# Kernel optimization log

Measured on AMD Instinct MI355X. Metric: run time of the kernel, lower is better.

## Reference

```python
import jax, jax.numpy as jnp
import numpy as np

N_NODES = 100000
N_EDGES = 1600000
EMB_DIM = 128
BN_EPS = 1e-5


def setup_inputs() -> dict:
    key = jax.random.key(0)
    k = jax.random.split(key, 5)
    x = jax.random.normal(k[0], (N_NODES, EMB_DIM), dtype=jnp.float32)
    src = jax.random.randint(k[1], (N_EDGES,), 0, N_NODES)
    dst = jax.random.randint(k[2], (N_EDGES,), 0, N_NODES)
    W = jax.random.normal(k[3], (EMB_DIM, EMB_DIM), dtype=jnp.float32) / np.float32(np.sqrt(EMB_DIM))
    b = jnp.zeros((EMB_DIM,), dtype=jnp.float32)
    gamma = jnp.ones((EMB_DIM,), dtype=jnp.float32)
    beta = jnp.zeros((EMB_DIM,), dtype=jnp.float32)
    return {"x": x, "src": src, "dst": dst, "W": W, "b": b, "gamma": gamma, "beta": beta}


def reference(x, src, dst, W, b, gamma, beta):
    n = x.shape[0]
    ones = jnp.ones(src.shape, dtype=x.dtype)
    # DGL GraphConv norm='both': degrees clamped to min 1
    deg_out = jnp.maximum(jax.ops.segment_sum(ones, src, num_segments=n), 1.0)
    deg_in = jnp.maximum(jax.ops.segment_sum(ones, dst, num_segments=n), 1.0)
    norm_src = jax.lax.rsqrt(deg_out)  # [N]
    norm_dst = jax.lax.rsqrt(deg_in)   # [N]
    # W applied before aggregation (in_feats == out_feats path in DGL)
    h = (x * norm_src[:, None]) @ W                              # [N, D]
    agg = jax.ops.segment_sum(h[src], dst, num_segments=n)       # SpMM gather/scatter, [N, D]
    h = agg * norm_dst[:, None] + b                              # [N, D]
    # BatchNorm1d over nodes (training-mode batch stats, biased variance)
    mean = jnp.mean(h, axis=0)
    var = jnp.var(h, axis=0)
    h = (h - mean) * jax.lax.rsqrt(var + BN_EPS) * gamma + beta
    h = jax.nn.relu(h)
    # dropout: identity in eval-mode reference
    return h + x  # residual
```

## Files before the change

### kernel.cpp

```cpp
#include <hip/hip_runtime.h>
#include <hip/hip_bf16.h>

#define NN 100000
#define NE 1600000
#define D  128
#define BN_EPS 1e-5f

#define CB  782
#define NC  256
#define EPC (NE / NC)
#define NSLICE  2
#define SLICESZ 61600
#define SW      (SLICESZ / 4)
#define SCH     256
#define EPH (NE / SCH)

#define GB   ((NN + 63) / 64)
#define SMB  ((NSLICE * SW + 255) / 256)

typedef __attribute__((ext_vector_type(8))) short bf16x8;
typedef __attribute__((ext_vector_type(4))) float f32x4;

#define WLD 136

static __device__ __forceinline__ ushort f2bf(float f) {
    __hip_bfloat16 b = __float2bfloat16(f);
    return *reinterpret_cast<ushort*>(&b);
}
static __device__ __forceinline__ float bflo(unsigned v) {
    return __uint_as_float((v & 0xffffu) << 16);
}
static __device__ __forceinline__ float bfhi(unsigned v) {
    return __uint_as_float(v & 0xffff0000u);
}

__global__ __launch_bounds__(256) void k_front(const int* __restrict__ src,
                                               const int* __restrict__ dst,
                                               const float* __restrict__ W,
                                               ushort* __restrict__ WT,
                                               int* __restrict__ SP,
                                               int* __restrict__ P,
                                               float* __restrict__ stats) {
    __shared__ int hist[SW];
    __shared__ int dh[CB];
    const int t = threadIdx.x;
    const int s = blockIdx.x >> 8;
    const int c = blockIdx.x & 255;
    for (int i = t; i < SW; i += 256) hist[i] = 0;
    for (int i = t; i < CB; i += 256) dh[i] = 0;
    __syncthreads();

    const int lo = s * SLICESZ;
    const int base = c * EPH;
    for (int i = t; i < EPH; i += 256) {
        int k = src[base + i] - lo;
        if ((unsigned)k < (unsigned)SLICESZ)
            atomicAdd(&hist[k >> 2], 1 << ((k & 3) * 8));
    }
    if (s == 0) {
        for (int i = t; i < EPH; i += 256)
            atomicAdd(&dh[dst[base + i] >> 7], 1);
    }
    __syncthreads();

    int* outS = SP + (size_t)blockIdx.x * SW;
    for (int i = t; i < SW; i += 256) outS[i] = hist[i];
    if (s == 0)
        for (int i = t; i < CB; i += 256) P[i * NC + c] = dh[i];
    if (s == 1 && c < 64) {
        int i = c * 256 + t;
        int n = i >> 7, k2 = i & 127;
        WT[i] = f2bf(W[k2 * D + n]);
    }
    if (s == 1 && c == 64) stats[t] = 0.0f;
}

__global__ __launch_bounds__(256) void k_mid(int* __restrict__ P,
                                             int* __restrict__ bintotal,
                                             const int* __restrict__ SP,
                                             float* __restrict__ degout) {
    const int t = threadIdx.x;
    if (blockIdx.x < CB) {
        __shared__ int sh[NC];
        const int b = blockIdx.x;
        const int v = P[b * NC + t];
        sh[t] = v;
        __syncthreads();
        for (int off = 1; off < NC; off <<= 1) {
            int u = (t >= off) ? sh[t - off] : 0;
            __syncthreads();
            sh[t] += u;
            __syncthreads();
        }
        P[b * NC + t] = sh[t] - v;
        if (t == NC - 1) bintotal[b] = sh[t];
    } else {
        int w = (blockIdx.x - CB) * 256 + t;
        if (w >= NSLICE * SW) return;
        const int s = w / SW, wi = w - s * SW;
        const int n0 = s * SLICESZ + wi * 4;
        if (n0 >= NN) return;
        const int* col = SP + (size_t)s * SCH * SW + wi;
        int b0 = 0, b1 = 0, b2 = 0, b3 = 0;
#pragma unroll 8
        for (int c = 0; c < SCH; ++c) {
            unsigned v = (unsigned)col[(size_t)c * SW];
            b0 += v & 0xFF;
            b1 += (v >> 8) & 0xFF;
            b2 += (v >> 16) & 0xFF;
            b3 += (v >> 24);
        }
        degout[n0] = (float)b0;
        if (n0 + 1 < NN) degout[n0 + 1] = (float)b1;
        if (n0 + 2 < NN) degout[n0 + 2] = (float)b2;
        if (n0 + 3 < NN) degout[n0 + 3] = (float)b3;
    }
}

__global__ __launch_bounds__(1024) void k_cscanB(const int* __restrict__ bintotal,
                                                 int* __restrict__ binbase) {
    __shared__ int sh[1024];
    const int t = threadIdx.x;
    const int v = (t < CB) ? bintotal[t] : 0;
    sh[t] = v;
    __syncthreads();
    for (int off = 1; off < 1024; off <<= 1) {
        int u = (t >= off) ? sh[t - off] : 0;
        __syncthreads();
        sh[t] += u;
        __syncthreads();
    }
    if (t < CB) binbase[t] = sh[t] - v;
    if (t == CB - 1) binbase[CB] = sh[t];
}

__global__ __launch_bounds__(256) void k_cscatter(const int* __restrict__ dst,
                                                  const int* __restrict__ src,
                                                  const int* __restrict__ P,
                                                  const int* __restrict__ binbase,
                                                  int* __restrict__ sedge) {
    __shared__ int cur[CB];
    const int c = blockIdx.x;
    const int t = threadIdx.x;
    for (int i = t; i < CB; i += 256) cur[i] = binbase[i] + P[i * NC + c];
    __syncthreads();
    const int base = c * EPC;
    for (int i = t; i < EPC; i += 256) {
        int d = dst[base + i];
        int pos = atomicAdd(&cur[d >> 7], 1);
        sedge[pos] = src[base + i] | ((d & 127) << 17);
    }
}

__global__ __launch_bounds__(256) void k_gf(const float* __restrict__ x,
                                            const float* __restrict__ degout,
                                            const ushort* __restrict__ WT,
                                            ushort* __restrict__ h,
                                            const int* __restrict__ sedge,
                                            const int* __restrict__ binbase,
                                            int* __restrict__ ptr,
                                            int* __restrict__ esrc) {
    __shared__ ushort Wl[D * WLD];
    __shared__ int fh[128], fp[128], fcur[128];
    const int t = threadIdx.x;

    if (blockIdx.x < GB) {
        for (int s = t; s < 2048; s += 256) {
            int row = s >> 4, slot = s & 15;
            uint4 v = *reinterpret_cast<const uint4*>(WT + row * D + slot * 8);
            *reinterpret_cast<uint4*>(&Wl[row * WLD + slot * 8]) = v;
        }
        __syncthreads();

        const int wave = t >> 6;
        const int lane = t & 63;
        const int m16  = lane & 15;
        const int kq   = lane >> 4;
        const int row  = blockIdx.x * 64 + wave * 16 + m16;
        const int rc   = row < NN ? row : NN - 1;

        const float nrm = rsqrtf(fmaxf(degout[rc], 1.0f));

        bf16x8 afrag[4];
        const float* xr = x + (size_t)rc * D + kq * 8;
#pragma unroll
        for (int kt = 0; kt < 4; ++kt) {
            f32x4 lo = *reinterpret_cast<const f32x4*>(xr + kt * 32);
            f32x4 hi = *reinterpret_cast<const f32x4*>(xr + kt * 32 + 4);
            union { bf16x8 v; ushort u[8]; } af;
#pragma unroll
            for (int j = 0; j < 4; ++j) {
                af.u[j]     = f2bf(lo[j] * nrm);
                af.u[4 + j] = f2bf(hi[j] * nrm);
            }
            afrag[kt] = af.v;
        }

        f32x4 acc[8];
#pragma unroll
        for (int nt = 0; nt < 8; ++nt) acc[nt] = (f32x4)(0.0f);

#pragma unroll
        for (int kt = 0; kt < 4; ++kt) {
#pragma unroll
            for (int nt = 0; nt < 8; ++nt) {
                int n = nt * 16 + m16;
                const bf16x8 bfrag = *reinterpret_cast<const bf16x8*>(
                    &Wl[n * WLD + kt * 32 + kq * 8]);
                acc[nt] = __builtin_amdgcn_mfma_f32_16x16x32_bf16(afrag[kt], bfrag, acc[nt], 0, 0, 0);
            }
        }

        const int orow = blockIdx.x * 64 + wave * 16 + kq * 4;
#pragma unroll
        for (int nt = 0; nt < 8; ++nt) {
#pragma unroll
            for (int r = 0; r < 4; ++r) {
                int rr = orow + r;
                if (rr < NN) h[(size_t)rr * D + nt * 16 + m16] = f2bf(acc[nt][r]);
            }
        }
    } else {
        const int b = blockIdx.x - GB;
        const int lo = binbase[b], hi = binbase[b + 1];
        if (t < 128) fh[t] = 0;
        __syncthreads();
        for (int i = lo + t; i < hi; i += 256)
            atomicAdd(&fh[(unsigned)sedge[i] >> 17], 1);
        __syncthreads();
        if (t < 128) fp[t] = fh[t];
        __syncthreads();
        for (int off = 1; off < 128; off <<= 1) {
            int u = (t < 128 && t >= off) ? fp[t - off] : 0;
            __syncthreads();
            if (t < 128) fp[t] += u;
            __syncthreads();
        }
        if (t < 128) {
            const int node = b * 128 + t;
            const int ex = fp[t] - fh[t];
            fcur[t] = ex;
            if (node < NN) {
                ptr[node] = lo + ex;
            } else if (node == NN) {
                ptr[NN] = lo + ex;
            }
        }
        __syncthreads();
        for (int i = lo + t; i < hi; i += 256) {
            unsigned v = (unsigned)sedge[i];
            int pos = atomicAdd(&fcur[v >> 17], 1);
            esrc[lo + pos] = v & 0x1FFFF;
        }
    }
}

__global__ __launch_bounds__(256) void k_agg(const ushort* __restrict__ h,
                                             const int* __restrict__ ptr,
                                             const int* __restrict__ esrc,
                                             const float* __restrict__ b,
                                             ushort* __restrict__ h2) {
    const int node = blockIdx.x * 4 + (threadIdx.x >> 6);
    const int lane = threadIdx.x & 63;
    if (node >= NN) return;
    const int s0 = ptr[node];
    const int s1 = ptr[node + 1];
    const int eg = lane >> 4;
    const int cb = (lane & 15) * 8;

    float acc[8];
#pragma unroll
    for (int j = 0; j < 8; ++j) acc[j] = 0.0f;

    for (int i = s0; i < s1; i += 16) {
        int  idx[4];
        bool p[4];
        uint4 v[4];
#pragma unroll
        for (int u = 0; u < 4; ++u) {
            int ii = i + eg + 4 * u;
            p[u] = ii < s1;
            if (p[u]) idx[u] = esrc[ii];
        }
#pragma unroll
        for (int u = 0; u < 4; ++u)
            if (p[u]) v[u] = *reinterpret_cast<const uint4*>(h + (size_t)idx[u] * D + cb);
#pragma unroll
        for (int u = 0; u < 4; ++u) {
            if (p[u]) {
                acc[0] += bflo(v[u].x); acc[1] += bfhi(v[u].x);
                acc[2] += bflo(v[u].y); acc[3] += bfhi(v[u].y);
                acc[4] += bflo(v[u].z); acc[5] += bfhi(v[u].z);
                acc[6] += bflo(v[u].w); acc[7] += bfhi(v[u].w);
            }
        }
    }
#pragma unroll
    for (int j = 0; j < 8; ++j) {
        acc[j] += __shfl_xor(acc[j], 16, 64);
        acc[j] += __shfl_xor(acc[j], 32, 64);
    }
    if (eg == 0) {
        const float nrm = rsqrtf(fmaxf((float)(s1 - s0), 1.0f));
        uint4 o;
        unsigned w[4];
#pragma unroll
        for (int m = 0; m < 4; ++m) {
            float e0 = acc[2 * m]     * nrm + b[cb + 2 * m];
            float e1 = acc[2 * m + 1] * nrm + b[cb + 2 * m + 1];
            w[m] = (unsigned)f2bf(e0) | ((unsigned)f2bf(e1) << 16);
        }
        o.x = w[0]; o.y = w[1]; o.z = w[2]; o.w = w[3];
        *reinterpret_cast<uint4*>(h2 + (size_t)node * D + cb) = o;
    }
}

__global__ __launch_bounds__(256) void k_stats(const unsigned* __restrict__ h2u,
                                               float* __restrict__ stats) {
    __shared__ float red[4][256];
    const int t = threadIdx.x;
    float s1lo = 0.f, s1hi = 0.f, s2lo = 0.f, s2hi = 0.f;
    const int total = NN * (D / 2);
    const int stride = gridDim.x * 256;
    for (int i = blockIdx.x * 256 + t; i < total; i += stride) {
        unsigned v = h2u[i];
        float lo = bflo(v), hi = bfhi(v);
        s1lo += lo; s1hi += hi;
        s2lo += lo * lo; s2hi += hi * hi;
    }
    red[0][t] = s1lo; red[1][t] = s1hi; red[2][t] = s2lo; red[3][t] = s2hi;
    __syncthreads();
    if (t < 64) {
        const int c = t * 2;
        float a0 = red[0][t] + red[0][t + 64] + red[0][t + 128] + red[0][t + 192];
        float a1 = red[1][t] + red[1][t + 64] + red[1][t + 128] + red[1][t + 192];
        float q0 = red[2][t] + red[2][t + 64] + red[2][t + 128] + red[2][t + 192];
        float q1 = red[3][t] + red[3][t + 64] + red[3][t + 128] + red[3][t + 192];
        atomicAdd(&stats[c], a0);
        atomicAdd(&stats[c + 1], a1);
        atomicAdd(&stats[128 + c], q0);
        atomicAdd(&stats[128 + c + 1], q1);
    }
}

__global__ void k_final(const uint2* __restrict__ h2v, const float4* __restrict__ xv,
                        const float* __restrict__ gamma, const float* __restrict__ beta,
                        const float* __restrict__ stats, float4* __restrict__ outv) {
    const int i = blockIdx.x * 256 + threadIdx.x;
    const int total = NN * (D / 4);
    if (i >= total) return;
    const int c = (i & 31) * 4;
    const float inv_n = 1.0f / (float)NN;
    uint2 v = h2v[i];
    float4 xx = xv[i];
    float hv[4] = { bflo(v.x), bfhi(v.x), bflo(v.y), bfhi(v.y) };
    float xr[4] = { xx.x, xx.y, xx.z, xx.w };
    float o[4];
#pragma unroll
    for (int m = 0; m < 4; ++m) {
        float mean = stats[c + m] * inv_n;
        float var  = stats[128 + c + m] * inv_n - mean * mean;
        float t = (hv[m] - mean) * rsqrtf(var + BN_EPS) * gamma[c + m] + beta[c + m];
        o[m] = fmaxf(t, 0.0f) + xr[m];
    }
    float4 ov; ov.x = o[0]; ov.y = o[1]; ov.z = o[2]; ov.w = o[3];
    outv[i] = ov;
}

extern "C" void kernel_launch(void* const* d_in, const int* in_sizes, int n_in,
                              void* d_out, int out_size, void* d_ws, size_t ws_size,
                              hipStream_t stream) {
    const float* x     = (const float*)d_in[0];
    const int*   src   = (const int*)d_in[1];
    const int*   dst   = (const int*)d_in[2];
    const float* W     = (const float*)d_in[3];
    const float* b     = (const float*)d_in[4];
    const float* gamma = (const float*)d_in[5];
    const float* beta  = (const float*)d_in[6];
    float* out = (float*)d_out;

    float* ws     = (float*)d_ws;
    ushort* h2    = (ushort*)ws;
    float* degout = ws + (size_t)NN * D;
    float* stats  = degout + NN;
    int*   ptr    = (int*)(stats + 256);
    int*   esrc   = ptr + (NN + 1);
    ushort* WT    = (ushort*)(esrc + NE);

    int* sedge    = (int*)ws;
    int* SP       = sedge + NE;
    int* P        = SP + (size_t)NSLICE * SCH * SW;
    int* bintotal = P + (size_t)CB * NC;
    int* binbase  = bintotal + CB;

    ushort* h = (ushort*)d_out;

    k_front<<<NSLICE * SCH, 256, 0, stream>>>(src, dst, W, WT, SP, P, stats);
    k_mid<<<CB + SMB, 256, 0, stream>>>(P, bintotal, SP, degout);
    k_cscanB<<<1, 1024, 0, stream>>>(bintotal, binbase);
    k_cscatter<<<NC, 256, 0, stream>>>(dst, src, P, binbase, sedge);
    k_gf<<<GB + CB, 256, 0, stream>>>(x, degout, WT, h, sedge, binbase, ptr, esrc);
    k_agg<<<(NN + 3) / 4, 256, 0, stream>>>(h, ptr, esrc, b, h2);
    k_stats<<<1024, 256, 0, stream>>>((const unsigned*)h2, stats);
    k_final<<<(NN * (D / 4) + 255) / 256, 256, 0, stream>>>((const uint2*)h2, (const float4*)x,
                                                            gamma, beta, stats, (float4*)out);
}
```

Measured before the change: 226.2 us.

## Fuse bin scan into coarse scatter and overlap scatter with GEMM blocks

```diff
diff --git a/kernel.cpp b/kernel.cpp
--- a/kernel.cpp
+++ b/kernel.cpp
@@ -117,51 +117,20 @@
     }
 }
 
-__global__ __launch_bounds__(1024) void k_cscanB(const int* __restrict__ bintotal,
-                                                 int* __restrict__ binbase) {
-    __shared__ int sh[1024];
-    const int t = threadIdx.x;
-    const int v = (t < CB) ? bintotal[t] : 0;
-    sh[t] = v;
-    __syncthreads();
-    for (int off = 1; off < 1024; off <<= 1) {
-        int u = (t >= off) ? sh[t - off] : 0;
-        __syncthreads();
-        sh[t] += u;
-        __syncthreads();
-    }
-    if (t < CB) binbase[t] = sh[t] - v;
-    if (t == CB - 1) binbase[CB] = sh[t];
-}
-
-__global__ __launch_bounds__(256) void k_cscatter(const int* __restrict__ dst,
-                                                  const int* __restrict__ src,
-                                                  const int* __restrict__ P,
-                                                  const int* __restrict__ binbase,
-                                                  int* __restrict__ sedge) {
+__global__ __launch_bounds__(256) void k_csg(const float* __restrict__ x,
+                                             const float* __restrict__ degout,
+                                             const ushort* __restrict__ WT,
+                                             ushort* __restrict__ h,
+                                             const int* __restrict__ dst,
+                                             const int* __restrict__ src,
+                                             const int* __restrict__ P,
+                                             const int* __restrict__ bintotal,
+                                             int* __restrict__ binbase,
+                                             int* __restrict__ sedge) {
+    __shared__ ushort Wl[D * WLD];
+    __shared__ int part[256];
+    __shared__ int bb[CB];
     __shared__ int cur[CB];
-    const int c = blockIdx.x;
-    const int t = threadIdx.x;
-    for (int i = t; i < CB; i += 256) cur[i] = binbase[i] + P[i * NC + c];
-    __syncthreads();
-    const int base = c * EPC;
-    for (int i = t; i < EPC; i += 256) {
-        int d = dst[base + i];
-        int pos = atomicAdd(&cur[d >> 7], 1);
-        sedge[pos] = src[base + i] | ((d & 127) << 17);
-    }
-}
-
-__global__ __launch_bounds__(256) void k_gf(const float* __restrict__ x,
-                                            const float* __restrict__ degout,
-                                            const ushort* __restrict__ WT,
-                                            ushort* __restrict__ h,
-                                            const int* __restrict__ sedge,
-                                            const int* __restrict__ binbase,
-                                            int* __restrict__ ptr,
-                                            int* __restrict__ esrc) {
-    __shared__ ushort Wl[D * WLD];
-    __shared__ int fh[128], fp[128], fcur[128];
     const int t = threadIdx.x;
 
     if (blockIdx.x < GB) {
@@ -221,37 +190,82 @@
             }
         }
     } else {
-        const int b = blockIdx.x - GB;
-        const int lo = binbase[b], hi = binbase[b + 1];
-        if (t < 128) fh[t] = 0;
-        __syncthreads();
-        for (int i = lo + t; i < hi; i += 256)
-            atomicAdd(&fh[(unsigned)sedge[i] >> 17], 1);
-        __syncthreads();
-        if (t < 128) fp[t] = fh[t];
-        __syncthreads();
-        for (int off = 1; off < 128; off <<= 1) {
-            int u = (t < 128 && t >= off) ? fp[t - off] : 0;
+        const int c = blockIdx.x - GB;
+        int val[4];
+        int sum = 0;
+#pragma unroll
+        for (int j = 0; j < 4; ++j) {
+            int idx = t * 4 + j;
+            val[j] = (idx < CB) ? bintotal[idx] : 0;
+            sum += val[j];
+        }
+        part[t] = sum;
+        __syncthreads();
+        for (int off = 1; off < 256; off <<= 1) {
+            int u = (t >= off) ? part[t - off] : 0;
             __syncthreads();
-            if (t < 128) fp[t] += u;
+            part[t] += u;
             __syncthreads();
         }
-        if (t < 128) {
-            const int node = b * 128 + t;
-            const int ex = fp[t] - fh[t];
-            fcur[t] = ex;
-            if (node < NN) {
-                ptr[node] = lo + ex;
-            } else if (node == NN) {
-                ptr[NN] = lo + ex;
-            }
-        }
-        __syncthreads();
-        for (int i = lo + t; i < hi; i += 256) {
-            unsigned v = (unsigned)sedge[i];
-            int pos = atomicAdd(&fcur[v >> 17], 1);
-            esrc[lo + pos] = v & 0x1FFFF;
-        }
+        int run = (t == 0) ? 0 : part[t - 1];
+#pragma unroll
+        for (int j = 0; j < 4; ++j) {
+            int idx = t * 4 + j;
+            if (idx < CB) bb[idx] = run;
+            run += val[j];
+        }
+        __syncthreads();
+        if (c == 0) {
+            for (int i = t; i < CB; i += 256) binbase[i] = bb[i];
+            if (t == 0) binbase[CB] = part[255];
+        }
+        for (int i = t; i < CB; i += 256) cur[i] = bb[i] + P[i * NC + c];
+        __syncthreads();
+        const int base = c * EPC;
+        for (int i = t; i < EPC; i += 256) {
+            int d = dst[base + i];
+            int pos = atomicAdd(&cur[d >> 7], 1);
+            sedge[pos] = src[base + i] | ((d & 127) << 17);
+        }
+    }
+}
+
+__global__ __launch_bounds__(256) void k_fine(const int* __restrict__ sedge,
+                                              const int* __restrict__ binbase,
+                                              int* __restrict__ ptr,
+                                              int* __restrict__ esrc) {
+    __shared__ int fh[128], fp[128], fcur[128];
+    const int b = blockIdx.x;
+    const int t = threadIdx.x;
+    const int lo = binbase[b], hi = binbase[b + 1];
+    if (t < 128) fh[t] = 0;
+    __syncthreads();
+    for (int i = lo + t; i < hi; i += 256)
+        atomicAdd(&fh[(unsigned)sedge[i] >> 17], 1);
+    __syncthreads();
+    if (t < 128) fp[t] = fh[t];
+    __syncthreads();
+    for (int off = 1; off < 128; off <<= 1) {
+        int u = (t < 128 && t >= off) ? fp[t - off] : 0;
+        __syncthreads();
+        if (t < 128) fp[t] += u;
+        __syncthreads();
+    }
+    if (t < 128) {
+        const int node = b * 128 + t;
+        const int ex = fp[t] - fh[t];
+        fcur[t] = ex;
+        if (node < NN) {
+            ptr[node] = lo + ex;
+        } else if (node == NN) {
+            ptr[NN] = lo + ex;
+        }
+    }
+    __syncthreads();
+    for (int i = lo + t; i < hi; i += 256) {
+        unsigned v = (unsigned)sedge[i];
+        int pos = atomicAdd(&fcur[v >> 17], 1);
+        esrc[lo + pos] = v & 0x1FFFF;
     }
 }
 
@@ -397,9 +411,8 @@
 
     k_front<<<NSLICE * SCH, 256, 0, stream>>>(src, dst, W, WT, SP, P, stats);
     k_mid<<<CB + SMB, 256, 0, stream>>>(P, bintotal, SP, degout);
-    k_cscanB<<<1, 1024, 0, stream>>>(bintotal, binbase);
-    k_cscatter<<<NC, 256, 0, stream>>>(dst, src, P, binbase, sedge);
-    k_gf<<<GB + CB, 256, 0, stream>>>(x, degout, WT, h, sedge, binbase, ptr, esrc);
+    k_csg<<<GB + NC, 256, 0, stream>>>(x, degout, WT, h, dst, src, P, bintotal, binbase, sedge);
+    k_fine<<<CB, 256, 0, stream>>>(sedge, binbase, ptr, esrc);
     k_agg<<<(NN + 3) / 4, 256, 0, stream>>>(h, ptr, esrc, b, h2);
     k_stats<<<1024, 256, 0, stream>>>((const unsigned*)h2, stats);
     k_final<<<(NN * (D / 4) + 255) / 256, 256, 0, stream>>>((const uint2*)h2, (const float4*)x,
```

Result: no change. 224.9 us (median of 2 runs) (-0.6%).
